# Optimization experiments

Hardware: AMD Instinct MI355X
Metric: run time of the kernel (lower is better)

The kernel has to match this reference:

```python
import jax, jax.numpy as jnp
import numpy as np


def _hemisphere(radius=1.0, n=5):
    # replicates DiffuseShader.generate_hemisphere with sample=(5j,5j)
    u, v = np.mgrid[0:np.pi:n * 1j, 0:np.pi:n * 1j]
    x = (radius * np.cos(u) * np.sin(v)).flatten()
    y = (radius * np.sin(u) * np.sin(v)).flatten()
    z = (radius * np.cos(v)).flatten()
    return jnp.asarray(np.c_[x, y, z], dtype=jnp.float32)


def _diffuse_forward(V, COL, OPA, p, l, normals, hemi_vecs, indices, pointindex):
    P, S, N = p.shape[0], hemi_vecs.shape[0], V.shape[0]
    local = pointindex % P
    # --- project_hemisphere_projection: Rodrigues rotation local->global ---
    u = l[None, :] - p                                      # [P,3]
    u_hat = u / jnp.linalg.norm(u, axis=1, keepdims=True)
    v_loc = jnp.broadcast_to(jnp.array([0.0, -1.0, 0.0], p.dtype), u_hat.shape)
    c = -u_hat[:, 1:2]                                      # rowwise dot(v_loc, u_hat), [P,1]
    w = jnp.cross(v_loc, u_hat)                             # [P,3]
    z0 = jnp.zeros_like(w[:, 0])
    vmat = jnp.stack([jnp.stack([z0, -w[:, 2], w[:, 1]], -1),
                      jnp.stack([w[:, 2], z0, -w[:, 0]], -1),
                      jnp.stack([-w[:, 1], w[:, 0], z0], -1)], axis=1)  # [P,3,3] skew(w)
    R = jnp.eye(3, dtype=p.dtype)[None] + vmat + jnp.matmul(vmat, vmat) / (1.0 + c)[..., None]
    lh = jnp.einsum('pij,sj->psi', R, hemi_vecs) + l        # [P,S,3]
    o = jnp.broadcast_to(p[:, None, :], (P, S, 3))
    d = lh - o
    # --- get_intersection: ray/plane distances ---
    nrm = jnp.cross(V[:, 1] - V[:, 0], V[:, 2] - V[:, 0])
    nrm = nrm / jnp.linalg.norm(nrm, axis=1, keepdims=True)  # [N,3]
    kk = -jnp.sum(nrm * V[:, 3], axis=1)                     # [N]
    vo = o.reshape(P * S, 3) @ nrm.T                         # [P*S,N]
    vd = d.reshape(P * S, 3) @ nrm.T
    t = (-(kk[None, :] + vo) / vd).reshape(P, N, S)          # faithful to torch .view(P,N,S) on the [P*S,N] buffer
    surf = indices[pointindex, 0]
    mat = indices[pointindex, 1]
    empty = jnp.zeros((P, N, S), bool).at[local, surf, :].set(True)
    viable = (t > -1e-4) & (t < 1.0) & (~empty)
    # --- barycentric condition test ---
    r = o[:, None, :, :] + t[..., None] * d[:, None, :, :]   # [P,N,S,3]
    a0 = V[:, 0, 0][None, :, None]; a1 = V[:, 0, 1][None, :, None]; a2 = V[:, 0, 2][None, :, None]
    b0 = V[:, 1, 0][None, :, None]; b1 = V[:, 1, 1][None, :, None]; b2 = V[:, 1, 2][None, :, None]
    c0 = V[:, 2, 0][None, :, None]; c1 = V[:, 2, 1][None, :, None]; c2 = V[:, 2, 2][None, :, None]
    r0, r1, r2 = r[..., 0], r[..., 1], r[..., 2]
    A = a0 * r2 - a2 * r0
    B = a0 * b2 - a2 * b0
    C = a0 * r1 - a1 * r0
    D = a0 * b1 - a1 * b0
    E = a0 * c2 - a2 * c0
    F = B * (a1 * c0 - a0 * c1)
    gam = (D * (A * D - B * C)) / (D * (E * D + F))
    beta = (C + gam * (a1 * c0 - a0 * c1)) / D
    alpha = (r0 - (beta * b0 + gam * c0)) / a0
    mask = jnp.where(viable & (beta > 0.0) & (gam > 0.0) & (alpha > 0.0), 1.0, 0.0).astype(jnp.float32)
    col = COL[surf, mat]                                     # [P,3]
    opa = jnp.clip(OPA[surf, mat], 0.0, 1.0)                 # [P]
    reflected_ray = l[None, :] - p                           # [P,3]
    return mask, col, opa, reflected_ray


def setup_inputs() -> dict:
    P, N, M, G = 512, 1024, 8, 2048
    key = jax.random.key(0)
    ks = jax.random.split(key, 8)
    V = jax.random.normal(ks[0], (N, 4, 3), jnp.float32)
    indices = jax.random.randint(ks[1], (G, 2), 0, M)
    pointindex = jax.random.randint(ks[2], (P,), 0, G)
    COL = jax.random.uniform(ks[3], (N, M, 3), jnp.float32)
    OPA = jax.random.uniform(ks[4], (N, M), jnp.float32)
    p = jax.random.normal(ks[5], (P, 3), jnp.float32) * 5.0
    l = jax.random.normal(ks[6], (3,), jnp.float32) * 10.0 + 20.0
    normals = jax.random.normal(ks[7], (N, 3), jnp.float32)
    return {"V": V, "indices": indices, "pointindex": pointindex, "COL": COL,
            "OPA": OPA, "p": p, "l": l, "normals": normals, "it": 0,
            "hemi_vecs": _hemisphere(1.0, 5)}


def reference(V, indices, pointindex, COL, OPA, p, l, normals, it, hemi_vecs):
    return _diffuse_forward(V, COL, OPA, p, l, normals, hemi_vecs, indices, pointindex)
```

## Files before the change

### kernel.cpp

```cpp
#include <hip/hip_runtime.h>
#include <math.h>

#define NP   512
#define NT   1024
#define NS   25
#define NPS  (NP*NS)
#define MASKN (NP*NT*NS)

#define DSA_OFF  0
#define PD_OFF   51200
#define NX_OFF   53248
#define NY_OFF   54272
#define NZ_OFF   55296
#define KK_OFF   56320
#define W_OFF    57344
#define EMPTY_OFF ((size_t)67584 * 8)

__device__ __forceinline__ double sgn(double x) {
    return (x > 0.0) ? 1.0 : ((x < 0.0) ? -1.0 : 0.0);
}

__global__ void prep_all(const float* __restrict__ p,
                         const float* __restrict__ l,
                         const float* __restrict__ hemi,
                         const float* __restrict__ V,
                         const int* __restrict__ indices,
                         const int* __restrict__ pointindex,
                         const float* __restrict__ COL,
                         const float* __restrict__ OPA,
                         double* __restrict__ ws,
                         unsigned* __restrict__ emptyMask,
                         float* __restrict__ out) {
    const int b = blockIdx.x, t = threadIdx.x;
    if (b < 50) {
        int idx = b * 256 + t;
        int pi = idx / NS, si = idx % NS;
        double px = p[pi*3+0], py = p[pi*3+1], pz = p[pi*3+2];
        double lx = l[0], ly = l[1], lz = l[2];
        double ux = lx - px, uy = ly - py, uz = lz - pz;
        double nrm = sqrt(ux*ux + uy*uy + uz*uz);
        ux /= nrm; uy /= nrm; uz /= nrm;
        double c = -uy;
        double wx = -uz, wz = ux;
        double m01 = -wz, m10 = wz, m12 = -wx, m21 = wx;
        double q00 = m01*m10;
        double q02 = m01*m12;
        double q11 = m10*m01 + m12*m21;
        double q20 = m21*m10;
        double q22 = m21*m12;
        double ic = 1.0 + c;
        double r00 = 1.0 + q00/ic, r01 = m01,            r02 = q02/ic;
        double r10 = m10,          r11 = 1.0 + q11/ic,   r12 = m12;
        double r20 = q20/ic,       r21 = m21,            r22 = 1.0 + q22/ic;
        double hx = hemi[si*3+0], hy = hemi[si*3+1], hz = hemi[si*3+2];
        double lhx = r00*hx + r01*hy + r02*hz + lx;
        double lhy = r10*hx + r11*hy + r12*hz + ly;
        double lhz = r20*hx + r21*hy + r22*hz + lz;
        double* dsA = ws + DSA_OFF;
        dsA[idx*4+0] = lhx - px;
        dsA[idx*4+1] = lhy - py;
        dsA[idx*4+2] = lhz - pz;
        dsA[idx*4+3] = 0.0;
    } else if (b < 54) {
        int n = (b - 50) * 256 + t;
        const float* v = V + n*12;
        double a0=v[0], a1=v[1], a2=v[2];
        double b0=v[3], b1=v[4], b2=v[5];
        double c0=v[6], c1=v[7], c2=v[8];
        double v3x=v[9], v3y=v[10], v3z=v[11];
        double e1x=b0-a0, e1y=b1-a1, e1z=b2-a2;
        double e2x=c0-a0, e2y=c1-a1, e2z=c2-a2;
        double cx = e1y*e2z - e1z*e2y;
        double cy = e1z*e2x - e1x*e2z;
        double cz = e1x*e2y - e1y*e2x;
        double nn = sqrt(cx*cx + cy*cy + cz*cz);
        double nx = cx/nn, ny = cy/nn, nz = cz/nn;
        double kk = -(nx*v3x + ny*v3y + nz*v3z);
        double Bv = a0*b2 - a2*b0;
        double Dv = a0*b1 - a1*b0;
        double Ec = a0*c2 - a2*c0;
        double G2 = a1*c0 - a0*c1;
        double Fc = Bv*G2;
        double gd = Dv*(Ec*Dv + Fc);
        double gq = Dv*gd;
        double dq = Dv*c0;
        double aq = a0*gq;
        double WGr0 = a1*Bv - a2*Dv, WGr1 = -(a0*Bv), WGr2 = a0*Dv;
        double dg = Dv*G2;
        double WBr0 = -(a1*gd) + dg*WGr0;
        double WBr1 =  a0*gd  + dg*WGr1;
        double WBr2 =            dg*WGr2;
        double dd = Dv*dq;
        double WAr0 = gq - b0*WBr0 - dd*WGr0;
        double WAr1 =    - b0*WBr1 - dd*WGr1;
        double WAr2 =    - b0*WBr2 - dd*WGr2;
        double sg = sgn(Dv*gd), sb = sgn(gq), sa = sgn(aq);
        ws[NX_OFF + n] = nx;
        ws[NY_OFF + n] = ny;
        ws[NZ_OFF + n] = nz;
        ws[KK_OFF + n] = kk;
        double* W = ws + W_OFF + n*10;
        W[0] = WGr0*sg; W[1] = WGr1*sg; W[2] = WGr2*sg;
        W[3] = WBr0*sb; W[4] = WBr1*sb; W[5] = WBr2*sb;
        W[6] = WAr0*sa; W[7] = WAr1*sa; W[8] = WAr2*sa;
        W[9] = 0.0;
    } else {
        emptyMask[t] = 0u;
        emptyMask[t + 256] = 0u;
        __syncthreads();
        for (int i = t; i < NP; i += 256) {
            int pidx = pointindex[i];
            int local = pidx & (NP - 1);
            int surf = indices[pidx*2 + 0];
            int mat  = indices[pidx*2 + 1];
            atomicOr(&emptyMask[local], 1u << surf);
            float* colOut = out + MASKN;
            float* opaOut = out + MASKN + 3*NP;
            float* refOut = out + MASKN + 4*NP;
            colOut[i*3+0] = COL[(surf*8+mat)*3+0];
            colOut[i*3+1] = COL[(surf*8+mat)*3+1];
            colOut[i*3+2] = COL[(surf*8+mat)*3+2];
            float o = OPA[surf*8+mat];
            opaOut[i] = fminf(fmaxf(o, 0.0f), 1.0f);
            refOut[i*3+0] = (float)((double)l[0] - (double)p[i*3+0]);
            refOut[i*3+1] = (float)((double)l[1] - (double)p[i*3+1]);
            refOut[i*3+2] = (float)((double)l[2] - (double)p[i*3+2]);
            double* pd = ws + PD_OFF;
            pd[i*4+0] = (double)p[i*3+0];
            pd[i*4+1] = (double)p[i*3+1];
            pd[i*4+2] = (double)p[i*3+2];
            pd[i*4+3] = 0.0;
        }
    }
}

template<bool HE>
__device__ __forceinline__ void line_body(
        const double (*sW)[11],
        const double* sdx, const double* sdy, const double* sdz,
        double sx, double sy, double sz, double ox, double oy, double oz,
        const double2& nxa, const double2& nxb, const double2& nya, const double2& nyb,
        const double2& nza, const double2& nzb, const double2& kka, const double2& kkb,
        unsigned em, unsigned nn0, unsigned q, unsigned ps, unsigned tid,
        float* __restrict__ out) {
    const unsigned n0 = tid * 4u;
    const unsigned rem0 = (q << 10) + n0;
    unsigned nnk = rem0 / 25u;
    unsigned ssk = rem0 - nnk * 25u;

    float res[4];
    #pragma unroll
    for (int k = 0; k < 4; ++k) {
        const double nxv = (k < 2) ? (k ? nxa.y : nxa.x) : (k == 3 ? nxb.y : nxb.x);
        const double nyv = (k < 2) ? (k ? nya.y : nya.x) : (k == 3 ? nyb.y : nyb.x);
        const double nzv = (k < 2) ? (k ? nza.y : nza.x) : (k == 3 ? nzb.y : nzb.x);
        const double kkv = (k < 2) ? (k ? kka.y : kka.x) : (k == 3 ? kkb.y : kkb.x);

        const double vd = fma(sz, nzv, fma(sy, nyv, sx * nxv));
        const double tt = fma(oz, nzv, fma(oy, nyv, fma(ox, nxv, kkv)));
        const double e1 = fma(1e-4, vd, -tt);
        const double e2 = vd + tt;

        const double dxv = sdx[ssk], dyv = sdy[ssk], dzv = sdz[ssk];
        const double R0 = fma(-tt, dxv, vd * ox);
        const double R1 = fma(-tt, dyv, vd * oy);
        const double R2 = fma(-tt, dzv, vd * oz);

        const double* w = sW[nnk - nn0];
        const double dG = fma(R2, w[2], fma(R1, w[1], R0 * w[0]));
        const double dB = fma(R2, w[5], fma(R1, w[4], R0 * w[3]));
        const double dA = fma(R2, w[8], fma(R1, w[7], R0 * w[6]));

        const int hv = __double2hiint(vd);
        int m = (__double2hiint(e1) ^ hv) | (__double2hiint(e2) ^ hv)
              | (__double2hiint(dG) ^ hv) | (__double2hiint(dB) ^ hv)
              | (__double2hiint(dA) ^ hv);
        bool ok = (m >= 0);
        if (HE) ok = ok && !((nnk < 8u) && ((em >> nnk) & 1u));
        res[k] = ok ? 1.0f : 0.0f;

        ssk += 1u;
        const bool wrap = (ssk == 25u);
        nnk += wrap ? 1u : 0u;
        ssk  = wrap ? 0u : ssk;
    }
    *(float4*)(out + ps*1024u + n0) = make_float4(res[0], res[1], res[2], res[3]);
}

__global__ __launch_bounds__(256, 4) void diffuse_main(
        const double* __restrict__ ws,
        const unsigned* __restrict__ emptyMask,
        float* __restrict__ out) {
    __shared__ double sW[42][11];
    __shared__ double sdx[25], sdy[25], sdz[25];

    const unsigned ps = blockIdx.x;
    const unsigned pp = ps / 25u;
    const unsigned q  = ps - pp * 25u;
    const unsigned nn0 = (q << 10) / 25u;
    const unsigned tid = threadIdx.x;

    const unsigned n0 = tid * 4u;
    const double2 nxa = *(const double2*)(ws + NX_OFF + n0);
    const double2 nxb = *(const double2*)(ws + NX_OFF + n0 + 2);
    const double2 nya = *(const double2*)(ws + NY_OFF + n0);
    const double2 nyb = *(const double2*)(ws + NY_OFF + n0 + 2);
    const double2 nza = *(const double2*)(ws + NZ_OFF + n0);
    const double2 nzb = *(const double2*)(ws + NZ_OFF + n0 + 2);
    const double2 kka = *(const double2*)(ws + KK_OFF + n0);
    const double2 kkb = *(const double2*)(ws + KK_OFF + n0 + 2);
    const double sx = ws[DSA_OFF + ps*4u + 0];
    const double sy = ws[DSA_OFF + ps*4u + 1];
    const double sz = ws[DSA_OFF + ps*4u + 2];
    const double ox = ws[PD_OFF + pp*4u + 0];
    const double oy = ws[PD_OFF + pp*4u + 1];
    const double oz = ws[PD_OFF + pp*4u + 2];
    const unsigned em = (q == 0u) ? emptyMask[pp] : 0u;

    const double* Wg = ws + W_OFF;
    if (tid < 210u) {
        unsigned row = tid / 5u, col = tid - row * 5u;
        unsigned gn = nn0 + row; if (gn > 1023u) gn = 1023u;
        const double2 v = *(const double2*)(Wg + gn*10u + col*2u);
        sW[row][col*2u]   = v.x;
        sW[row][col*2u+1] = v.y;
    }
    if (tid < 25u) {
        const double* dr = ws + DSA_OFF + (pp*25u + tid)*4u;
        sdx[tid] = dr[0]; sdy[tid] = dr[1]; sdz[tid] = dr[2];
    }
    __syncthreads();

    if (q == 0u)
        line_body<true >(sW, sdx, sdy, sdz, sx, sy, sz, ox, oy, oz,
                         nxa, nxb, nya, nyb, nza, nzb, kka, kkb,
                         em, nn0, q, ps, tid, out);
    else
        line_body<false>(sW, sdx, sdy, sdz, sx, sy, sz, ox, oy, oz,
                         nxa, nxb, nya, nyb, nza, nzb, kka, kkb,
                         em, nn0, q, ps, tid, out);
}

extern "C" void kernel_launch(void* const* d_in, const int* in_sizes, int n_in,
                              void* d_out, int out_size, void* d_ws, size_t ws_size,
                              hipStream_t stream) {
    const float* V         = (const float*)d_in[0];
    const int*   indices   = (const int*)  d_in[1];
    const int*   pointindex= (const int*)  d_in[2];
    const float* COL       = (const float*)d_in[3];
    const float* OPA       = (const float*)d_in[4];
    const float* p         = (const float*)d_in[5];
    const float* l         = (const float*)d_in[6];
    const float* hemi      = (const float*)d_in[9];

    float* out = (float*)d_out;
    double* ws = (double*)d_ws;
    unsigned* emptyMask = (unsigned*)((char*)d_ws + EMPTY_OFF);

    prep_all<<<55, 256, 0, stream>>>(p, l, hemi, V, indices, pointindex,
                                     COL, OPA, ws, emptyMask, out);
    diffuse_main<<<NPS, 256, 0, stream>>>(ws, emptyMask, out);
}
```

Before: 40.16 us.

## Run intersection test in fp32 with error-bounded fallback to fp64 recheck

Prep now also writes fp32 copies of ray directions, origins, plane normals/offsets and row-normalized barycentric weights. The main kernel evaluates the sign tests in fp32 and computes conservative error bounds per element. Only when a quantity is within the bound of zero does it recompute that element in fp64 from the workspace. This targets the low fp64 throughput and register pressure, at the cost of extra prep writes, divergent fallback paths and reliance on the error bound being truly conservative.

```diff
diff --git a/kernel.cpp b/kernel.cpp
--- a/kernel.cpp
+++ b/kernel.cpp
@@ -15,6 +15,16 @@
 #define KK_OFF   56320
 #define W_OFF    57344
 #define EMPTY_OFF ((size_t)67584 * 8)
+#define F32_BYTE_OFF (EMPTY_OFF + 2048)
+#define FD_OFF   0
+#define FPD_OFF  51200
+#define FNX_OFF  53248
+#define FNY_OFF  54272
+#define FNZ_OFF  55296
+#define FKK_OFF  56320
+#define FW_OFF   57344
+
+#define CEPS 7.6293945e-06f
 
 __device__ __forceinline__ double sgn(double x) {
     return (x > 0.0) ? 1.0 : ((x < 0.0) ? -1.0 : 0.0);
@@ -32,6 +42,7 @@
                          unsigned* __restrict__ emptyMask,
                          float* __restrict__ out) {
     const int b = blockIdx.x, t = threadIdx.x;
+    float* __restrict__ f32w = (float*)((char*)ws + F32_BYTE_OFF);
     if (b < 50) {
         int idx = b * 256 + t;
         int pi = idx / NS, si = idx % NS;
@@ -53,14 +64,16 @@
         double r10 = m10,          r11 = 1.0 + q11/ic,   r12 = m12;
         double r20 = q20/ic,       r21 = m21,            r22 = 1.0 + q22/ic;
         double hx = hemi[si*3+0], hy = hemi[si*3+1], hz = hemi[si*3+2];
-        double lhx = r00*hx + r01*hy + r02*hz + lx;
-        double lhy = r10*hx + r11*hy + r12*hz + ly;
-        double lhz = r20*hx + r21*hy + r22*hz + lz;
+        double dx = r00*hx + r01*hy + r02*hz + lx - px;
+        double dy = r10*hx + r11*hy + r12*hz + ly - py;
+        double dz = r20*hx + r21*hy + r22*hz + lz - pz;
         double* dsA = ws + DSA_OFF;
-        dsA[idx*4+0] = lhx - px;
-        dsA[idx*4+1] = lhy - py;
-        dsA[idx*4+2] = lhz - pz;
+        dsA[idx*4+0] = dx;
+        dsA[idx*4+1] = dy;
+        dsA[idx*4+2] = dz;
         dsA[idx*4+3] = 0.0;
+        *(float4*)(f32w + FD_OFF + idx*4) =
+            make_float4((float)dx, (float)dy, (float)dz, 0.0f);
     } else if (b < 54) {
         int n = (b - 50) * 256 + t;
         const float* v = V + n*12;
@@ -99,11 +112,27 @@
         ws[NY_OFF + n] = ny;
         ws[NZ_OFF + n] = nz;
         ws[KK_OFF + n] = kk;
+        double g0 = WGr0*sg, g1 = WGr1*sg, g2 = WGr2*sg;
+        double bb0 = WBr0*sb, bb1 = WBr1*sb, bb2 = WBr2*sb;
+        double aa0 = WAr0*sa, aa1 = WAr1*sa, aa2 = WAr2*sa;
         double* W = ws + W_OFF + n*10;
-        W[0] = WGr0*sg; W[1] = WGr1*sg; W[2] = WGr2*sg;
-        W[3] = WBr0*sb; W[4] = WBr1*sb; W[5] = WBr2*sb;
-        W[6] = WAr0*sa; W[7] = WAr1*sa; W[8] = WAr2*sa;
-        W[9] = 0.0;
+        W[0]=g0; W[1]=g1; W[2]=g2;
+        W[3]=bb0; W[4]=bb1; W[5]=bb2;
+        W[6]=aa0; W[7]=aa1; W[8]=aa2;
+        W[9]=0.0;
+        f32w[FNX_OFF+n]=(float)nx; f32w[FNY_OFF+n]=(float)ny;
+        f32w[FNZ_OFF+n]=(float)nz; f32w[FKK_OFF+n]=(float)kk;
+        double wsg = fabs(g0)+fabs(g1)+fabs(g2);
+        double wsb = fabs(bb0)+fabs(bb1)+fabs(bb2);
+        double wsa = fabs(aa0)+fabs(aa1)+fabs(aa2);
+        double ig = wsg>0.0 ? 1.0/wsg : 0.0;
+        double ib = wsb>0.0 ? 1.0/wsb : 0.0;
+        double ia = wsa>0.0 ? 1.0/wsa : 0.0;
+        float* fw = f32w + FW_OFF + n*12;
+        fw[0]=(float)(g0*ig);  fw[1]=(float)(g1*ig);  fw[2]=(float)(g2*ig);
+        fw[3]=(float)(bb0*ib); fw[4]=(float)(bb1*ib); fw[5]=(float)(bb2*ib);
+        fw[6]=(float)(aa0*ia); fw[7]=(float)(aa1*ia); fw[8]=(float)(aa2*ia);
+        fw[9]=0.0f; fw[10]=0.0f; fw[11]=0.0f;
     } else {
         emptyMask[t] = 0u;
         emptyMask[t + 256] = 0u;
@@ -130,115 +159,138 @@
             pd[i*4+1] = (double)p[i*3+1];
             pd[i*4+2] = (double)p[i*3+2];
             pd[i*4+3] = 0.0;
+            *(float4*)(f32w + FPD_OFF + i*4) =
+                make_float4(p[i*3+0], p[i*3+1], p[i*3+2], 0.0f);
         }
     }
 }
 
-template<bool HE>
-__device__ __forceinline__ void line_body(
-        const double (*sW)[11],
-        const double* sdx, const double* sdy, const double* sdz,
-        double sx, double sy, double sz, double ox, double oy, double oz,
-        const double2& nxa, const double2& nxb, const double2& nya, const double2& nyb,
-        const double2& nza, const double2& nzb, const double2& kka, const double2& kkb,
-        unsigned em, unsigned nn0, unsigned q, unsigned ps, unsigned tid,
-        float* __restrict__ out) {
-    const unsigned n0 = tid * 4u;
-    const unsigned rem0 = (q << 10) + n0;
-    unsigned nnk = rem0 / 25u;
-    unsigned ssk = rem0 - nnk * 25u;
-
-    float res[4];
-    #pragma unroll
-    for (int k = 0; k < 4; ++k) {
-        const double nxv = (k < 2) ? (k ? nxa.y : nxa.x) : (k == 3 ? nxb.y : nxb.x);
-        const double nyv = (k < 2) ? (k ? nya.y : nya.x) : (k == 3 ? nyb.y : nyb.x);
-        const double nzv = (k < 2) ? (k ? nza.y : nza.x) : (k == 3 ? nzb.y : nzb.x);
-        const double kkv = (k < 2) ? (k ? kka.y : kka.x) : (k == 3 ? kkb.y : kkb.x);
-
-        const double vd = fma(sz, nzv, fma(sy, nyv, sx * nxv));
-        const double tt = fma(oz, nzv, fma(oy, nyv, fma(ox, nxv, kkv)));
-        const double e1 = fma(1e-4, vd, -tt);
-        const double e2 = vd + tt;
-
-        const double dxv = sdx[ssk], dyv = sdy[ssk], dzv = sdz[ssk];
-        const double R0 = fma(-tt, dxv, vd * ox);
-        const double R1 = fma(-tt, dyv, vd * oy);
-        const double R2 = fma(-tt, dzv, vd * oz);
-
-        const double* w = sW[nnk - nn0];
-        const double dG = fma(R2, w[2], fma(R1, w[1], R0 * w[0]));
-        const double dB = fma(R2, w[5], fma(R1, w[4], R0 * w[3]));
-        const double dA = fma(R2, w[8], fma(R1, w[7], R0 * w[6]));
-
-        const int hv = __double2hiint(vd);
-        int m = (__double2hiint(e1) ^ hv) | (__double2hiint(e2) ^ hv)
-              | (__double2hiint(dG) ^ hv) | (__double2hiint(dB) ^ hv)
-              | (__double2hiint(dA) ^ hv);
-        bool ok = (m >= 0);
-        if (HE) ok = ok && !((nnk < 8u) && ((em >> nnk) & 1u));
-        res[k] = ok ? 1.0f : 0.0f;
-
-        ssk += 1u;
-        const bool wrap = (ssk == 25u);
-        nnk += wrap ? 1u : 0u;
-        ssk  = wrap ? 0u : ssk;
-    }
-    *(float4*)(out + ps*1024u + n0) = make_float4(res[0], res[1], res[2], res[3]);
+__device__ __forceinline__ float recheck64(const double* __restrict__ ws,
+        unsigned ps, unsigned pp, unsigned i, unsigned nn, unsigned ss,
+        unsigned em) {
+    const double* s = ws + DSA_OFF + ps*4u;
+    const double* o = ws + PD_OFF + pp*4u;
+    double nx = ws[NX_OFF+i], ny = ws[NY_OFF+i], nz = ws[NZ_OFF+i];
+    double kk = ws[KK_OFF+i];
+    double vd = fma(s[2], nz, fma(s[1], ny, s[0]*nx));
+    double tt = fma(o[2], nz, fma(o[1], ny, fma(o[0], nx, kk)));
+    double e1 = fma(1e-4, vd, -tt);
+    double e2 = vd + tt;
+    const double* d = ws + DSA_OFF + (pp*25u + ss)*4u;
+    double R0 = fma(-tt, d[0], vd*o[0]);
+    double R1 = fma(-tt, d[1], vd*o[1]);
+    double R2 = fma(-tt, d[2], vd*o[2]);
+    const double* w = ws + W_OFF + nn*10u;
+    double dG = fma(R2, w[2], fma(R1, w[1], R0*w[0]));
+    double dB = fma(R2, w[5], fma(R1, w[4], R0*w[3]));
+    double dA = fma(R2, w[8], fma(R1, w[7], R0*w[6]));
+    int hv = __double2hiint(vd);
+    int m = (__double2hiint(e1)^hv) | (__double2hiint(e2)^hv)
+          | (__double2hiint(dG)^hv) | (__double2hiint(dB)^hv)
+          | (__double2hiint(dA)^hv);
+    bool ok = (m >= 0) && !((nn < 8u) && ((em >> nn) & 1u));
+    return ok ? 1.0f : 0.0f;
 }
 
 __global__ __launch_bounds__(256, 4) void diffuse_main(
         const double* __restrict__ ws,
         const unsigned* __restrict__ emptyMask,
         float* __restrict__ out) {
-    __shared__ double sW[42][11];
-    __shared__ double sdx[25], sdy[25], sdz[25];
-
+    __shared__ float sW[42][12];
+    __shared__ float sdx[25], sdy[25], sdz[25], sdm[25];
+
+    const float* __restrict__ f32 = (const float*)((const char*)ws + F32_BYTE_OFF);
     const unsigned ps = blockIdx.x;
     const unsigned pp = ps / 25u;
-    const unsigned q  = ps - pp * 25u;
+    const unsigned q  = ps - pp*25u;
     const unsigned nn0 = (q << 10) / 25u;
     const unsigned tid = threadIdx.x;
-
     const unsigned n0 = tid * 4u;
-    const double2 nxa = *(const double2*)(ws + NX_OFF + n0);
-    const double2 nxb = *(const double2*)(ws + NX_OFF + n0 + 2);
-    const double2 nya = *(const double2*)(ws + NY_OFF + n0);
-    const double2 nyb = *(const double2*)(ws + NY_OFF + n0 + 2);
-    const double2 nza = *(const double2*)(ws + NZ_OFF + n0);
-    const double2 nzb = *(const double2*)(ws + NZ_OFF + n0 + 2);
-    const double2 kka = *(const double2*)(ws + KK_OFF + n0);
-    const double2 kkb = *(const double2*)(ws + KK_OFF + n0 + 2);
-    const double sx = ws[DSA_OFF + ps*4u + 0];
-    const double sy = ws[DSA_OFF + ps*4u + 1];
-    const double sz = ws[DSA_OFF + ps*4u + 2];
-    const double ox = ws[PD_OFF + pp*4u + 0];
-    const double oy = ws[PD_OFF + pp*4u + 1];
-    const double oz = ws[PD_OFF + pp*4u + 2];
+
+    const float4 fnx = *(const float4*)(f32 + FNX_OFF + n0);
+    const float4 fny = *(const float4*)(f32 + FNY_OFF + n0);
+    const float4 fnz = *(const float4*)(f32 + FNZ_OFF + n0);
+    const float4 fkk = *(const float4*)(f32 + FKK_OFF + n0);
+    const float sx = f32[FD_OFF + ps*4u + 0];
+    const float sy = f32[FD_OFF + ps*4u + 1];
+    const float sz = f32[FD_OFF + ps*4u + 2];
+    const float ox = f32[FPD_OFF + pp*4u + 0];
+    const float oy = f32[FPD_OFF + pp*4u + 1];
+    const float oz = f32[FPD_OFF + pp*4u + 2];
     const unsigned em = (q == 0u) ? emptyMask[pp] : 0u;
-
-    const double* Wg = ws + W_OFF;
-    if (tid < 210u) {
-        unsigned row = tid / 5u, col = tid - row * 5u;
+    const float S1u = fabsf(sx) + fabsf(sy) + fabsf(sz);
+    const float O1u = fabsf(ox) + fabsf(oy) + fabsf(oz);
+    const float Evd = CEPS * S1u;
+    const float Eb0 = S1u + O1u;
+    const float SOu = S1u * O1u;
+
+    if (tid < 126u) {
+        unsigned row = tid / 3u, quad = tid - row*3u;
         unsigned gn = nn0 + row; if (gn > 1023u) gn = 1023u;
-        const double2 v = *(const double2*)(Wg + gn*10u + col*2u);
-        sW[row][col*2u]   = v.x;
-        sW[row][col*2u+1] = v.y;
+        const float4 v = *(const float4*)(f32 + FW_OFF + gn*12u + quad*4u);
+        *(float4*)(&sW[row][quad*4u]) = v;
     }
     if (tid < 25u) {
-        const double* dr = ws + DSA_OFF + (pp*25u + tid)*4u;
-        sdx[tid] = dr[0]; sdy[tid] = dr[1]; sdz[tid] = dr[2];
+        const float4 dr = *(const float4*)(f32 + FD_OFF + (pp*25u + tid)*4u);
+        sdx[tid] = dr.x; sdy[tid] = dr.y; sdz[tid] = dr.z;
+        sdm[tid] = fmaxf(fabsf(dr.x), fmaxf(fabsf(dr.y), fabsf(dr.z)));
     }
     __syncthreads();
 
-    if (q == 0u)
-        line_body<true >(sW, sdx, sdy, sdz, sx, sy, sz, ox, oy, oz,
-                         nxa, nxb, nya, nyb, nza, nzb, kka, kkb,
-                         em, nn0, q, ps, tid, out);
-    else
-        line_body<false>(sW, sdx, sdy, sdz, sx, sy, sz, ox, oy, oz,
-                         nxa, nxb, nya, nyb, nza, nzb, kka, kkb,
-                         em, nn0, q, ps, tid, out);
+    const float nxk[4] = {fnx.x, fnx.y, fnx.z, fnx.w};
+    const float nyk[4] = {fny.x, fny.y, fny.z, fny.w};
+    const float nzk[4] = {fnz.x, fnz.y, fnz.z, fnz.w};
+    const float kkk[4] = {fkk.x, fkk.y, fkk.z, fkk.w};
+
+    unsigned rem = (q << 10) + n0;
+    unsigned nn = rem / 25u;
+    unsigned ss = rem - nn*25u;
+
+    float res[4];
+    #pragma unroll
+    for (int k = 0; k < 4; ++k) {
+        const float nx = nxk[k], ny = nyk[k], nz = nzk[k], kk = kkk[k];
+        const float vd = fmaf(sz, nz, fmaf(sy, ny, sx*nx));
+        const float tt = fmaf(oz, nz, fmaf(oy, ny, fmaf(ox, nx, kk)));
+        const float e1 = fmaf(1e-4f, vd, -tt);
+        const float e2 = vd + tt;
+
+        const float dxv = sdx[ss], dyv = sdy[ss], dzv = sdz[ss], dmv = sdm[ss];
+        const float R0 = fmaf(-tt, dxv, vd*ox);
+        const float R1 = fmaf(-tt, dyv, vd*oy);
+        const float R2 = fmaf(-tt, dzv, vd*oz);
+
+        const float* w = sW[nn - nn0];
+        const float dG = fmaf(R2, w[2], fmaf(R1, w[1], R0*w[0]));
+        const float dB = fmaf(R2, w[5], fmaf(R1, w[4], R0*w[3]));
+        const float dA = fmaf(R2, w[8], fmaf(R1, w[7], R0*w[6]));
+
+        const int hv = __float_as_int(vd);
+        int msk = (__float_as_int(e1)^hv) | (__float_as_int(e2)^hv)
+                | (__float_as_int(dG)^hv) | (__float_as_int(dB)^hv)
+                | (__float_as_int(dA)^hv);
+        bool ok = (msk >= 0) && !((nn < 8u) && ((em >> nn) & 1u));
+
+        const float akk = fabsf(kk);
+        const float Ee  = CEPS * (Eb0 + akk);
+        const float Mtt = O1u + akk;
+        const float MR  = fmaf(Mtt, dmv, SOu);
+        const float Edx = CEPS * MR;
+        const float mind = fminf(fabsf(dG), fminf(fabsf(dB), fabsf(dA)));
+        const bool flag = (fabsf(vd) < Evd) | (fabsf(e1) < Ee)
+                        | (fabsf(e2) < Ee) | (mind < Edx);
+
+        float r = ok ? 1.0f : 0.0f;
+        if (__builtin_expect(flag, 0))
+            r = recheck64(ws, ps, pp, n0 + (unsigned)k, nn, ss, em);
+        res[k] = r;
+
+        ss += 1u;
+        const bool wrap = (ss == 25u);
+        nn += wrap ? 1u : 0u;
+        ss  = wrap ? 0u : ss;
+    }
+    *(float4*)(out + (ps << 10) + n0) = make_float4(res[0], res[1], res[2], res[3]);
 }
 
 extern "C" void kernel_launch(void* const* d_in, const int* in_sizes, int n_in,
```

New measurement: 33.65 us, median of 2. -16.2%, faster.
